# Kernel optimization log

Measured on AMD Instinct MI355X. Metric: run time of the kernel, lower is better.

## Reference

```python
import jax, jax.numpy as jnp
import numpy as np

B, IN_N, OUT_N, SEQ, FEAT = 8, 8, 8, 256, 64
GRID_SIZE, SPLINE_ORDER, KSIZE = 96, 3, 15
NC = GRID_SIZE + SPLINE_ORDER  # 99 coefficients


def _layer_norm(x, eps=1e-5):
    m = jnp.mean(x, axis=-1, keepdims=True)
    v = jnp.var(x, axis=-1, keepdims=True)
    return (x - m) / jnp.sqrt(v + eps)


def setup_inputs():
    key = jax.random.key(0)
    ks = jax.random.split(key, 8)
    x_in = jax.random.normal(ks[0], (B, IN_N, SEQ, FEAT), jnp.float32)
    proj_x_prev = jax.random.normal(ks[1], (B, IN_N, SEQ, FEAT), jnp.float32)
    grid = jnp.linspace(-1.0, 1.0, NC).astype(jnp.float32)
    lin = jnp.linspace(-1.0, 1.0, NC).astype(jnp.float32)
    spline_weights = jnp.broadcast_to(lin[None, None, :], (IN_N, OUT_N, NC)) \
        + 0.01 * jax.random.normal(ks[2], (IN_N, OUT_N, NC), jnp.float32)
    tau = 0.1 * jax.random.normal(ks[3], (IN_N, OUT_N), jnp.float32) + 0.1
    temperature = jnp.array(1.0, jnp.float32)
    omiga = jnp.full((IN_N, OUT_N), 0.2, jnp.float32)
    lim = float(np.sqrt(6.0 / (FEAT + FEAT)))  # xavier_uniform for W2
    W2s = jax.random.uniform(ks[4], (OUT_N, FEAT, FEAT), jnp.float32, -lim, lim)
    bs = jnp.zeros((OUT_N, SEQ, FEAT), jnp.float32)
    ln_w = jnp.ones((OUT_N, FEAT), jnp.float32)
    ln_b = jnp.zeros((OUT_N, FEAT), jnp.float32)
    alphas = jnp.ones((OUT_N,), jnp.float32)
    betas = jnp.ones((OUT_N,), jnp.float32)
    thetas = jnp.ones((OUT_N,), jnp.float32)
    gammas = jnp.ones((OUT_N,), jnp.float32)
    kb = float(1.0 / np.sqrt(1 * KSIZE))  # torch conv default init bound
    convk = jax.random.uniform(ks[5], (OUT_N, FEAT, 1, KSIZE), jnp.float32, -kb, kb)
    return dict(x_in=x_in, proj_x_prev=proj_x_prev, grid=grid,
                spline_weights=spline_weights, tau=tau, temperature=temperature,
                omiga=omiga, W2s=W2s, bs=bs, ln_w=ln_w, ln_b=ln_b,
                alphas=alphas, betas=betas, thetas=thetas, gammas=gammas,
                convk=convk)


def reference(x_in, proj_x_prev, grid, spline_weights, tau, temperature, omiga,
              W2s, bs, ln_w, ln_b, alphas, betas, thetas, gammas, convk):
    b, in_n, seq, feat = x_in.shape
    nc = grid.shape[0]
    # InstanceNorm1d: normalize over seq per (b, in_n, feat) channel, eps=1e-5
    mu = jnp.mean(x_in, axis=2, keepdims=True)
    var = jnp.var(x_in, axis=2, keepdims=True)
    x_norm = (x_in - mu) / jnp.sqrt(var + 1e-5)
    x_norm = jnp.clip(x_norm * 0.5, -0.99, 0.99)
    # cubic B-spline basis: [b, in_n, seq, feat, nc]
    h = 2.0 / (nc - 1)
    dist = jnp.abs(x_norm[..., None] - grid) / h
    basis = jax.nn.relu(2.0 - dist) ** 3 / 6.0 - jax.nn.relu(1.0 - dist) ** 3 * (4.0 / 6.0)
    spline_mapping = jnp.einsum('binfc,ioc->bionf', basis, spline_weights)
    activated = spline_mapping + jnp.abs(omiga)[None, :, :, None, None] * x_in[:, :, None]
    t_val = jnp.abs(temperature) * np.sqrt(seq / 256.0) + 1e-4
    eye = jnp.eye(seq, dtype=x_in.dtype)
    outs, projs = [], []
    for j in range(OUT_N):
        edges = activated[:, :, j]                    # [b, in_n, seq, feat]
        energy = jnp.mean(edges ** 2, axis=(-1, -2))  # [b, in_n]
        e_sqrt = jnp.sqrt(energy + 1e-8)
        tau_j = jnp.abs(tau[:, j])[None, :]
        mask = jax.nn.sigmoid((e_sqrt - tau_j) / t_val)[..., None, None]
        # energy-weighted attention over previous projections
        mult = (e_sqrt / (tau_j + 1e-8))[..., None, None]
        wp = proj_x_prev * mult * mask                # [b, in_n, seq, d]
        K = wp[:, 0::2].transpose(0, 2, 1, 3).reshape(b, seq, -1)
        Q = wp[:, 1::2].transpose(0, 2, 1, 3).reshape(b, seq, -1)
        K, Q = _layer_norm(K), _layer_norm(Q)
        raw = jnp.einsum('bsd,btd->bst', K, Q)
        W1 = jax.nn.softmax(raw / (np.sqrt(K.shape[-1]) * t_val), axis=-1)
        combined = jnp.sum(edges * mask, axis=1)      # [b, seq, feat]
        # SplineWeightLayer j (residual_proj = Identity since dims match)
        xn = _layer_norm(combined) * ln_w[j] + ln_b[j]
        x_prime = xn @ W2s[j] + bs[j]                 # [b, seq, feat]
        w3 = jax.lax.conv_general_dilated(
            x_prime.transpose(0, 2, 1), convk[j], window_strides=(1,),
            padding=[(KSIZE // 2, KSIZE // 2)], feature_group_count=feat,
            dimension_numbers=('NCH', 'OIH', 'NCH')).transpose(0, 2, 1)
        attn_kernel = jnp.abs(betas[j]) * W1 + jnp.abs(alphas[j]) * eye[None]
        spatial = jnp.einsum('bst,btd->bsd', attn_kernel, x_prime) \
            + jnp.abs(thetas[j]) * w3
        outs.append(spatial + gammas[j] * combined)
        projs.append(x_prime)
    return jnp.stack(outs, axis=1), jnp.stack(projs, axis=1)
```

## Files before the change

kernel.cpp:

```cpp
#include <hip/hip_runtime.h>
#include <hip/hip_bf16.h>
#include <math.h>

typedef __hip_bfloat16 bf16;
__device__ __forceinline__ float b2f(bf16 v){ return __bfloat162float(v); }

#define SEQL 256
#define FEAT 64
#define NC 99
#define KS 15

#define OFF_MU    0
#define OFF_RSTD  4096
#define OFF_EN    8192
#define OFF_RS    9728
#define OFF_R2    26112
#define OFF_COMB  42496
#define OFF_D     1091072
#define OFF_ACT   3188224

#define OUT1_OFF  1048576

__global__ void __launch_bounds__(256)
k_pre(const float* __restrict__ x_in, const float* __restrict__ proj,
      float* __restrict__ ws){
    int g = blockIdx.x;
    int t = threadIdx.x;

    if (g < 64) {
        int bi = g;
        int f = t & 63, q = t >> 6;
        const float* xp = x_in + (size_t)bi * SEQL * FEAT;
        float s = 0.f, ss = 0.f;
        for (int k = 0; k < 64; ++k) {
            int sidx = q * 64 + k;
            float v = xp[sidx * FEAT + f];
            s += v; ss += v * v;
        }
        __shared__ float ls[256], lss[256];
        ls[t] = s; lss[t] = ss;
        __syncthreads();
        if (q == 0) {
            float S  = ls[f]  + ls[64+f]  + ls[128+f]  + ls[192+f];
            float SS = lss[f] + lss[64+f] + lss[128+f] + lss[192+f];
            float m = S * (1.f/256.f);
            float var = SS * (1.f/256.f) - m * m;
            ws[OFF_MU   + bi*64 + f] = m;
            ws[OFF_RSTD + bi*64 + f] = rsqrtf(var + 1e-5f);
        }
        if (bi == 0) {
            for (int k = t; k < 512; k += 256) ws[OFF_EN + k] = 0.f;
        }
    } else if (g < 128) {
        int bi = g - 64;
        int s = t;
        const float4* row = (const float4*)(proj + ((size_t)bi*SEQL + s)*FEAT);
        float s1 = 0.f, s2 = 0.f;
        #pragma unroll
        for (int k = 0; k < 16; ++k) {
            float4 v = row[k];
            s1 += v.x + v.y + v.z + v.w;
            s2 += v.x*v.x + v.y*v.y + v.z*v.z + v.w*v.w;
        }
        ws[OFF_RS + bi*SEQL + s] = s1;
        ws[OFF_R2 + bi*SEQL + s] = s2;
    } else {
        int g2 = g - 128;
        int bi2 = g2 >> 4, sq = g2 & 15;
        int b = bi2 >> 2, i2 = bi2 & 3;
        __shared__ float PK[16*64];
        const float4* pk = (const float4*)(proj + (((size_t)(b*8 + 2*i2))*SEQL + sq*16)*FEAT);
        ((float4*)PK)[t] = pk[t];
        float4 q[16];
        const float4* pq = (const float4*)(proj + (((size_t)(b*8 + 2*i2 + 1))*SEQL + t)*FEAT);
        #pragma unroll
        for (int k = 0; k < 16; ++k) q[k] = pq[k];
        __syncthreads();
        float* Dp = ws + OFF_D + (((size_t)bi2*SEQL) + sq*16)*SEQL + t;
        for (int s = 0; s < 16; ++s) {
            const float4* kr = (const float4*)(PK + s*64);
            float d = 0.f;
            #pragma unroll
            for (int k = 0; k < 16; ++k) {
                float4 kv = kr[k];
                float4 qv = q[k];
                d += kv.x*qv.x + kv.y*qv.y + kv.z*qv.z + kv.w*qv.w;
            }
            Dp[(size_t)s*SEQL] = d;
        }
    }
}

__global__ void __launch_bounds__(256)
k_act(const float* __restrict__ x_in, const float* __restrict__ sw,
      const float* __restrict__ omiga, float* __restrict__ ws){
    int g = blockIdx.x;
    int bi = g >> 6, sq = g & 63;
    int i = bi & 7;
    int t = threadIdx.x;
    int f = t & 63, sl = t >> 6;
    int s = sq*4 + sl;

    __shared__ float swl[8*NC];
    __shared__ float om8[8];
    for (int k = t; k < 8*NC; k += 256) swl[k] = sw[i*8*NC + k];
    if (t < 8) om8[t] = fabsf(omiga[i*8 + t]);
    __syncthreads();

    float x = x_in[((size_t)bi*SEQL + s)*FEAT + f];
    float xn = (x - ws[OFF_MU + bi*64 + f]) * ws[OFF_RSTD + bi*64 + f] * 0.5f;
    xn = fminf(fmaxf(xn, -0.99f), 0.99f);
    float u = (xn + 1.f) * 49.f;
    int ic0 = (int)floorf(u) - 1;
    float bas[4];
    int   cs[4];
    #pragma unroll
    for (int k = 0; k < 4; ++k) {
        int c = ic0 + k;
        float d = fabsf(u - (float)c);
        float r2 = fmaxf(2.f - d, 0.f);
        float r1 = fmaxf(1.f - d, 0.f);
        float bv = (r2*r2*r2 - 4.f*r1*r1*r1) * (1.f/6.f);
        bool ok = (c >= 0) && (c < NC);
        bas[k] = ok ? bv : 0.f;
        cs[k]  = ok ? c : 0;
    }

    bf16* actp = (bf16*)(ws + OFF_ACT);
    float en[8];
    #pragma unroll
    for (int j = 0; j < 8; ++j) {
        const float* swj = swl + j*NC;
        float sp = bas[0]*swj[cs[0]] + bas[1]*swj[cs[1]]
                 + bas[2]*swj[cs[2]] + bas[3]*swj[cs[3]];
        float a = sp + om8[j] * x;
        en[j] = a * a;
        actp[(((size_t)bi*8 + j)*SEQL + s)*FEAT + f] = __float2bfloat16(a);
    }

    int lane = t & 63, wv = t >> 6;
    #pragma unroll
    for (int o = 32; o > 0; o >>= 1)
        #pragma unroll
        for (int j = 0; j < 8; ++j) en[j] += __shfl_xor(en[j], o);
    __shared__ float red[4][8];
    if (lane == 0)
        #pragma unroll
        for (int j = 0; j < 8; ++j) red[wv][j] = en[j];
    __syncthreads();
    if (t < 8) {
        float tot = red[0][t] + red[1][t] + red[2][t] + red[3][t];
        atomicAdd(&ws[OFF_EN + bi*8 + t], tot);
    }
}

__device__ __forceinline__ void mask_mult(float EN, float ta, float tv,
                                          float& mask, float& mult){
    float es = sqrtf(EN * (1.f/16384.f) + 1e-8f);
    mask = 1.f / (1.f + expf(-(es - ta) / tv));
    mult = es / (ta + 1e-8f);
}

__global__ void __launch_bounds__(256)
k_cl2(const float* __restrict__ lnw, const float* __restrict__ lnb,
      const float* __restrict__ W2s, const float* __restrict__ bsb,
      const float* __restrict__ tau, const float* __restrict__ temp,
      float* __restrict__ ws, float* __restrict__ out){
    int g = blockIdx.x;
    int b = g >> 8, j = (g >> 5) & 7, sc = g & 31;
    int t = threadIdx.x;
    int f = t & 63, wv = t >> 6;

    __shared__ float W2l[4096];
    __shared__ float mkj[8];
    __shared__ float xl[4][64];
    {
        const float4* w4 = (const float4*)(W2s + (size_t)j*4096);
        float4* l4 = (float4*)W2l;
        for (int k = t; k < 1024; k += 256) l4[k] = w4[k];
    }
    if (t < 8) {
        float tv = fabsf(temp[0]) + 1e-4f;
        float mk, mu;
        mask_mult(ws[OFF_EN + (b*8 + t)*8 + j], fabsf(tau[t*8 + j]), tv, mk, mu);
        mkj[t] = mk;
    }
    __syncthreads();

    float lnwj = lnw[j*64 + f], lnbj = lnb[j*64 + f];
    const bf16* actp = (const bf16*)(ws + OFF_ACT);

    #pragma unroll
    for (int it = 0; it < 2; ++it) {
        int s = sc*8 + wv*2 + it;
        float comb = 0.f;
        #pragma unroll
        for (int i = 0; i < 8; ++i)
            comb += mkj[i] * b2f(actp[(((size_t)(b*8 + i)*8 + j)*SEQL + s)*FEAT + f]);
        ws[OFF_COMB + (((size_t)(b*8 + j))*SEQL + s)*FEAT + f] = comb;

        float sm_ = comb, sq_ = comb*comb;
        #pragma unroll
        for (int o = 32; o > 0; o >>= 1) { sm_ += __shfl_xor(sm_, o); sq_ += __shfl_xor(sq_, o); }
        float m = sm_ * (1.f/64.f);
        float var = sq_ * (1.f/64.f) - m*m;
        float xnj = (comb - m) * rsqrtf(var + 1e-5f) * lnwj + lnbj;
        xl[wv][f] = xnj;
        float acc = bsb[((size_t)j*SEQL + s)*FEAT + f];
        #pragma unroll 8
        for (int f2 = 0; f2 < 64; ++f2)
            acc += xl[wv][f2] * W2l[f2*64 + f];
        out[OUT1_OFF + (((size_t)(b*8 + j))*SEQL + s)*FEAT + f] = acc;
    }
}

__global__ void __launch_bounds__(256)
k_attn(const float* __restrict__ temp, const float* __restrict__ convk,
       const float* __restrict__ al, const float* __restrict__ be,
       const float* __restrict__ th, const float* __restrict__ ga,
       const float* __restrict__ tau,
       float* __restrict__ ws, const float* __restrict__ xpo_base,
       float* __restrict__ out){
    int g = blockIdx.x;
    int bj = g >> 5, sg = g & 31;
    int b = bj >> 3, j = bj & 7;
    int s0 = sg * 8;
    int t = threadIdx.x;
    int lane = t & 63, wv = t >> 6;

    __shared__ float wls[8][256];
    __shared__ float part[8][4][64];
    __shared__ float redm[4][8];
    __shared__ float reds[4][8];
    __shared__ float cKs[4], cQs[4], ccs[4];
    __shared__ float mKs[8], iKs[8];

    if (t < 4) {
        int iK = 2*t, iQ = iK + 1;
        float tv = fabsf(temp[0]) + 1e-4f;
        float mk, mu, mq, muq;
        mask_mult(ws[OFF_EN + (b*8 + iK)*8 + j], fabsf(tau[iK*8 + j]), tv, mk, mu);
        mask_mult(ws[OFF_EN + (b*8 + iQ)*8 + j], fabsf(tau[iQ*8 + j]), tv, mq, muq);
        float k_ = mk * mu, q_ = mq * muq;
        cKs[t] = k_; cQs[t] = q_; ccs[t] = k_ * q_;
    }
    __syncthreads();

    float mQ = 0.f, e2Q = 0.f;
    #pragma unroll
    for (int i2 = 0; i2 < 4; ++i2) {
        float c = cQs[i2];
        float rs = ws[OFF_RS + (b*8 + 2*i2 + 1)*SEQL + t];
        float r2 = ws[OFF_R2 + (b*8 + 2*i2 + 1)*SEQL + t];
        mQ += c * rs; e2Q += c*c * r2;
    }
    mQ *= (1.f/256.f); e2Q *= (1.f/256.f);
    float iQ = rsqrtf(e2Q - mQ*mQ + 1e-5f);

    if (t < 8) {
        int s = s0 + t;
        float mK = 0.f, e2K = 0.f;
        #pragma unroll
        for (int i2 = 0; i2 < 4; ++i2) {
            float c = cKs[i2];
            float rs = ws[OFF_RS + (b*8 + 2*i2)*SEQL + s];
            float r2 = ws[OFF_R2 + (b*8 + 2*i2)*SEQL + s];
            mK += c * rs; e2K += c*c * r2;
        }
        mK *= (1.f/256.f); e2K *= (1.f/256.f);
        mKs[t] = mK;
        iKs[t] = rsqrtf(e2K - mK*mK + 1e-5f);
    }
    __syncthreads();

    float tv = fabsf(temp[0]) + 1e-4f;
    float rscale = 1.f / (16.f * tv);
    float raw[8];
    #pragma unroll
    for (int r = 0; r < 8; ++r) {
        float d = 0.f;
        #pragma unroll
        for (int i2 = 0; i2 < 4; ++i2)
            d += ccs[i2] * ws[OFF_D + (((size_t)(b*4 + i2))*SEQL + s0 + r)*SEQL + t];
        raw[r] = (d - 256.f*mKs[r]*mQ) * (iKs[r]*iQ) * rscale;
    }

    float mx[8];
    #pragma unroll
    for (int r = 0; r < 8; ++r) mx[r] = raw[r];
    #pragma unroll
    for (int o = 32; o > 0; o >>= 1)
        #pragma unroll
        for (int r = 0; r < 8; ++r) mx[r] = fmaxf(mx[r], __shfl_xor(mx[r], o));
    if (lane == 0)
        #pragma unroll
        for (int r = 0; r < 8; ++r) redm[wv][r] = mx[r];
    __syncthreads();
    float ex[8], sm[8];
    #pragma unroll
    for (int r = 0; r < 8; ++r) {
        float M = fmaxf(fmaxf(redm[0][r], redm[1][r]), fmaxf(redm[2][r], redm[3][r]));
        ex[r] = expf(raw[r] - M);
        sm[r] = ex[r];
    }
    #pragma unroll
    for (int o = 32; o > 0; o >>= 1)
        #pragma unroll
        for (int r = 0; r < 8; ++r) sm[r] += __shfl_xor(sm[r], o);
    if (lane == 0)
        #pragma unroll
        for (int r = 0; r < 8; ++r) reds[wv][r] = sm[r];
    __syncthreads();
    #pragma unroll
    for (int r = 0; r < 8; ++r) {
        float S = reds[0][r] + reds[1][r] + reds[2][r] + reds[3][r];
        wls[r][t] = ex[r] / S;
    }
    __syncthreads();

    const float* xp = xpo_base + (size_t)bj*SEQL*FEAT;
    const float* cb = ws + OFF_COMB + (size_t)bj*SEQL*FEAT;

    int f = lane, qtr = wv;
    float acc[8] = {0.f,0.f,0.f,0.f,0.f,0.f,0.f,0.f};
    for (int k = 0; k < 64; ++k) {
        int trow = qtr*64 + k;
        float xv = xp[(size_t)trow*FEAT + f];
        #pragma unroll
        for (int r = 0; r < 8; ++r) acc[r] += wls[r][trow] * xv;
    }
    #pragma unroll
    for (int r = 0; r < 8; ++r) part[r][qtr][f] = acc[r];
    __syncthreads();

    {
        float ckf[KS];
        #pragma unroll
        for (int k = 0; k < KS; ++k) ckf[k] = convk[((size_t)j*64 + lane)*KS + k];
        float aa = fabsf(al[j]), ab = fabsf(be[j]);
        float at = fabsf(th[j]), gm = ga[j];
        #pragma unroll
        for (int it = 0; it < 2; ++it) {
            int r = wv*2 + it;
            int s = s0 + r;
            float attn = part[r][0][lane] + part[r][1][lane] + part[r][2][lane] + part[r][3][lane];
            float w3 = 0.f;
            #pragma unroll
            for (int k = 0; k < KS; ++k) {
                int s2 = s + k - 7;
                if (s2 >= 0 && s2 < SEQL) w3 += xp[(size_t)s2*FEAT + lane] * ckf[k];
            }
            float res = ab*attn + aa*xp[(size_t)s*FEAT + lane] + at*w3 + gm*cb[(size_t)s*FEAT + lane];
            out[((size_t)bj*SEQL + s)*FEAT + lane] = res;
        }
    }
}

extern "C" void kernel_launch(void* const* d_in, const int* in_sizes, int n_in,
                              void* d_out, int out_size, void* d_ws, size_t ws_size,
                              hipStream_t stream) {
    const float* x_in  = (const float*)d_in[0];
    const float* proj  = (const float*)d_in[1];
    const float* sw    = (const float*)d_in[3];
    const float* tau   = (const float*)d_in[4];
    const float* temp  = (const float*)d_in[5];
    const float* omiga = (const float*)d_in[6];
    const float* W2s   = (const float*)d_in[7];
    const float* bsb   = (const float*)d_in[8];
    const float* lnw   = (const float*)d_in[9];
    const float* lnb   = (const float*)d_in[10];
    const float* al    = (const float*)d_in[11];
    const float* be    = (const float*)d_in[12];
    const float* th    = (const float*)d_in[13];
    const float* ga    = (const float*)d_in[14];
    const float* ck    = (const float*)d_in[15];
    float* out = (float*)d_out;
    float* ws = (float*)d_ws;

    k_pre  <<<640,  256, 0, stream>>>(x_in, proj, ws);
    k_act  <<<4096, 256, 0, stream>>>(x_in, sw, omiga, ws);
    k_cl2  <<<2048, 256, 0, stream>>>(lnw, lnb, W2s, bsb, tau, temp, ws, out);
    k_attn <<<2048, 256, 0, stream>>>(temp, ck, al, be, th, ga, tau, ws,
                                      out + OUT1_OFF, out);
}
```

Baseline: 172.4 us.

## Replace energy atomics with per-block partials and transpose spline weights in LDS

k_act now writes each block's per-edge energy partial sum to its own slot instead of using atomicAdd. That removes atomic contention and the zeroing pass in k_pre, and the workspace offsets are enlarged to hold 64 partials per edge. The downstream kernels k_cl2 and k_attn reduce the 64 partials with wavefront shuffles before computing the mask. Spline weights are also stored transposed in shared memory so each basis index reads 8 outputs with two float4 loads instead of scattered scalar loads.

New measurement: 179.7 us. +4.2%, slower.

```diff
diff --git a/kernel.cpp b/kernel.cpp
--- a/kernel.cpp
+++ b/kernel.cpp
@@ -13,11 +13,11 @@
 #define OFF_MU    0
 #define OFF_RSTD  4096
 #define OFF_EN    8192
-#define OFF_RS    9728
-#define OFF_R2    26112
-#define OFF_COMB  42496
-#define OFF_D     1091072
-#define OFF_ACT   3188224
+#define OFF_RS    40960
+#define OFF_R2    57344
+#define OFF_COMB  73728
+#define OFF_D     1122304
+#define OFF_ACT   3219456
 
 #define OUT1_OFF  1048576
 
@@ -47,9 +47,6 @@
             float var = SS * (1.f/256.f) - m * m;
             ws[OFF_MU   + bi*64 + f] = m;
             ws[OFF_RSTD + bi*64 + f] = rsqrtf(var + 1e-5f);
-        }
-        if (bi == 0) {
-            for (int k = t; k < 512; k += 256) ws[OFF_EN + k] = 0.f;
         }
     } else if (g < 128) {
         int bi = g - 64;
@@ -101,9 +98,12 @@
     int f = t & 63, sl = t >> 6;
     int s = sq*4 + sl;
 
-    __shared__ float swl[8*NC];
+    __shared__ float swt[NC*8];
     __shared__ float om8[8];
-    for (int k = t; k < 8*NC; k += 256) swl[k] = sw[i*8*NC + k];
+    for (int k = t; k < NC*8; k += 256) {
+        int j = k & 7, c = k >> 3;
+        swt[k] = sw[i*8*NC + j*NC + c];
+    }
     if (t < 8) om8[t] = fabsf(omiga[i*8 + t]);
     __syncthreads();
 
@@ -112,8 +112,8 @@
     xn = fminf(fmaxf(xn, -0.99f), 0.99f);
     float u = (xn + 1.f) * 49.f;
     int ic0 = (int)floorf(u) - 1;
-    float bas[4];
-    int   cs[4];
+
+    float sp[8] = {0.f,0.f,0.f,0.f,0.f,0.f,0.f,0.f};
     #pragma unroll
     for (int k = 0; k < 4; ++k) {
         int c = ic0 + k;
@@ -122,18 +122,19 @@
         float r1 = fmaxf(1.f - d, 0.f);
         float bv = (r2*r2*r2 - 4.f*r1*r1*r1) * (1.f/6.f);
         bool ok = (c >= 0) && (c < NC);
-        bas[k] = ok ? bv : 0.f;
-        cs[k]  = ok ? c : 0;
+        bv = ok ? bv : 0.f;
+        int cc = ok ? c : 0;
+        const float4* w4 = (const float4*)(swt + cc*8);
+        float4 w0 = w4[0], w1 = w4[1];
+        sp[0] += bv*w0.x; sp[1] += bv*w0.y; sp[2] += bv*w0.z; sp[3] += bv*w0.w;
+        sp[4] += bv*w1.x; sp[5] += bv*w1.y; sp[6] += bv*w1.z; sp[7] += bv*w1.w;
     }
 
     bf16* actp = (bf16*)(ws + OFF_ACT);
     float en[8];
     #pragma unroll
     for (int j = 0; j < 8; ++j) {
-        const float* swj = swl + j*NC;
-        float sp = bas[0]*swj[cs[0]] + bas[1]*swj[cs[1]]
-                 + bas[2]*swj[cs[2]] + bas[3]*swj[cs[3]];
-        float a = sp + om8[j] * x;
+        float a = sp[j] + om8[j] * x;
         en[j] = a * a;
         actp[(((size_t)bi*8 + j)*SEQL + s)*FEAT + f] = __float2bfloat16(a);
     }
@@ -150,7 +151,7 @@
     __syncthreads();
     if (t < 8) {
         float tot = red[0][t] + red[1][t] + red[2][t] + red[3][t];
-        atomicAdd(&ws[OFF_EN + bi*8 + t], tot);
+        ws[OFF_EN + (bi*8 + t)*64 + sq] = tot;
     }
 }
 
@@ -179,11 +180,18 @@
         float4* l4 = (float4*)W2l;
         for (int k = t; k < 1024; k += 256) l4[k] = w4[k];
     }
-    if (t < 8) {
+    if (t < 64) {
         float tv = fabsf(temp[0]) + 1e-4f;
-        float mk, mu;
-        mask_mult(ws[OFF_EN + (b*8 + t)*8 + j], fabsf(tau[t*8 + j]), tv, mk, mu);
-        mkj[t] = mk;
+        for (int i = 0; i < 8; ++i) {
+            float v = ws[OFF_EN + ((b*8 + i)*8 + j)*64 + t];
+            #pragma unroll
+            for (int o = 32; o > 0; o >>= 1) v += __shfl_xor(v, o);
+            if (t == 0) {
+                float mk, mu;
+                mask_mult(v, fabsf(tau[i*8 + j]), tv, mk, mu);
+                mkj[i] = mk;
+            }
+        }
     }
     __syncthreads();
 
@@ -232,17 +240,26 @@
     __shared__ float part[8][4][64];
     __shared__ float redm[4][8];
     __shared__ float reds[4][8];
+    __shared__ float mm8[8];
     __shared__ float cKs[4], cQs[4], ccs[4];
     __shared__ float mKs[8], iKs[8];
 
+    if (t < 64) {
+        float tv = fabsf(temp[0]) + 1e-4f;
+        for (int i = 0; i < 8; ++i) {
+            float v = ws[OFF_EN + ((b*8 + i)*8 + j)*64 + t];
+            #pragma unroll
+            for (int o = 32; o > 0; o >>= 1) v += __shfl_xor(v, o);
+            if (t == 0) {
+                float mk, mu;
+                mask_mult(v, fabsf(tau[i*8 + j]), tv, mk, mu);
+                mm8[i] = mk * mu;
+            }
+        }
+    }
+    __syncthreads();
     if (t < 4) {
-        int iK = 2*t, iQ = iK + 1;
-        float tv = fabsf(temp[0]) + 1e-4f;
-        float mk, mu, mq, muq;
-        mask_mult(ws[OFF_EN + (b*8 + iK)*8 + j], fabsf(tau[iK*8 + j]), tv, mk, mu);
-        mask_mult(ws[OFF_EN + (b*8 + iQ)*8 + j], fabsf(tau[iQ*8 + j]), tv, mq, muq);
-        float k_ = mk * mu, q_ = mq * muq;
-        cKs[t] = k_; cQs[t] = q_; ccs[t] = k_ * q_;
+        cKs[t] = mm8[2*t]; cQs[t] = mm8[2*t + 1]; ccs[t] = mm8[2*t]*mm8[2*t+1];
     }
     __syncthreads();
 
```
